# Optimization experiments

Hardware: AMD Instinct MI355X
Metric: run time of the kernel (lower is better)

## Reference

```python
import jax, jax.numpy as jnp
import numpy as np

B, S, F, H = 2, 1024, 1024, 16  # H = n_heads arg; effective chunks Hc = F // H = 64, head_dim = H = 16


def _lin(x, w, b):
    # torch nn.Linear: y = x @ W^T + b, W has shape (out, in)
    return jnp.einsum('bsf,of->bso', x, w) + b


def setup_inputs() -> dict:
    key = jax.random.key(0)
    ks = jax.random.split(key, 16)
    sc = 0.02
    d = {'x': jax.random.normal(ks[0], (B, S, F), jnp.float32)}
    names = ['wq', 'wk', 'wv', 'vq', 'vk', 'vv', 'wo']
    for i, n in enumerate(names):
        d[n + '_w'] = jax.random.normal(ks[1 + 2 * i], (F, F), jnp.float32) * sc
        d[n + '_b'] = jax.random.normal(ks[2 + 2 * i], (F,), jnp.float32) * sc
    return d


def reference(x, wq_w, wq_b, wk_w, wk_b, wv_w, wv_b,
              vq_w, vq_b, vk_w, vk_b, vv_w, vv_b, wo_w, wo_b):
    b, s, f = x.shape
    hc = f // H  # number of chunks produced by torch.split(., n_heads, dim=-1)
    q = _lin(_lin(x, wq_w, wq_b), vq_w, vq_b)
    k = _lin(_lin(x, wk_w, wk_b), vk_w, vk_b)
    v = _lin(_lin(x, wv_w, wv_b), vv_w, vv_b)
    # split into hc chunks of size H along feature dim, concat on batch dim -> (hc, b, s, H)
    q = q.reshape(b, s, hc, H).transpose(2, 0, 1, 3)
    k = k.reshape(b, s, hc, H).transpose(2, 0, 1, 3)
    v = v.reshape(b, s, hc, H).transpose(2, 0, 1, 3)
    scale = jnp.sqrt(jnp.asarray(H, q.dtype))
    scores = jnp.einsum('cbqh,cbkh->cbqk', q, k) / scale  # (hc, b, s, s)
    attn = jax.nn.softmax(scores, axis=-1)
    o = jnp.einsum('cbqk,cbkh->cbqh', attn, v)  # (hc, b, s, H)
    # torch: view(H, b, s, f//H) then unsqueeze(-2).swapaxes(0,-2).reshape(b,s,f)
    o = o.reshape(H, b, s, hc).transpose(1, 2, 0, 3).reshape(b, s, f)
    return _lin(o, wo_w, wo_b)
```

## Files before the change

kernel.cpp:

```cpp
#include <hip/hip_runtime.h>
#include <hip/hip_bf16.h>
#include <stdint.h>

typedef __bf16 bf16_t;
typedef __bf16 bf16x8 __attribute__((ext_vector_type(8)));
typedef __bf16 bf16x4 __attribute__((ext_vector_type(4)));
typedef float f32x4 __attribute__((ext_vector_type(4)));
typedef float f32x16 __attribute__((ext_vector_type(16)));
typedef uint32_t u32x4 __attribute__((ext_vector_type(4)));

#define XN 2097152
#define WN 1048576

typedef __attribute__((address_space(1))) const uint8_t* gas_ptr;
typedef __attribute__((address_space(3))) uint8_t* las_ptr;

static __device__ __forceinline__ uint16_t bfbits(float f) {
    bf16_t b = (bf16_t)f;
    return __builtin_bit_cast(uint16_t, b);
}

__global__ void cast_all_k(const float* __restrict__ x,
    const float* __restrict__ w0, const float* __restrict__ w1, const float* __restrict__ w2,
    const float* __restrict__ w3, const float* __restrict__ w4, const float* __restrict__ w5,
    const float* __restrict__ w6, bf16_t* __restrict__ dst)
{
    const int TOTC = (XN + 7 * WN) / 4;
    for (int c = blockIdx.x * blockDim.x + threadIdx.x; c < TOTC; c += gridDim.x * blockDim.x) {
        int el = c * 4;
        const float* s;
        if (el < XN) {
            s = x + el;
        } else {
            int r = el - XN;
            int wi = r >> 20;
            int off = r & (WN - 1);
            const float* wp = (wi == 0) ? w0 : (wi == 1) ? w1 : (wi == 2) ? w2
                             : (wi == 3) ? w3 : (wi == 4) ? w4 : (wi == 5) ? w5 : w6;
            s = wp + off;
        }
        float4 f = *(const float4*)s;
        bf16x4 o = { (bf16_t)f.x, (bf16_t)f.y, (bf16_t)f.z, (bf16_t)f.w };
        *(bf16x4*)(dst + el) = o;
    }
}

#define QSCALE 0.36067376022224085f

template<int EPI>
__global__ __launch_bounds__(256)
void gemm128(const bf16_t* __restrict__ A0, const bf16_t* __restrict__ A1, const bf16_t* __restrict__ A2,
             const bf16_t* __restrict__ W0, const bf16_t* __restrict__ W1, const bf16_t* __restrict__ W2,
             const float* __restrict__ bias0, const float* __restrict__ bias1, const float* __restrict__ bias2,
             void* O0, void* O1, void* O2)
{
    const int z = blockIdx.z;
    const bf16_t* A = (z == 0) ? A0 : (z == 1) ? A1 : A2;
    const bf16_t* W = (z == 0) ? W0 : (z == 1) ? W1 : W2;
    const float* bias = (z == 0) ? bias0 : (z == 1) ? bias1 : bias2;
    void* Ov = (z == 0) ? O0 : (z == 1) ? O1 : O2;

    __shared__ bf16_t As[128 * 64];
    __shared__ bf16_t Bs[128 * 64];

    const int tid = threadIdx.x;
    const int lane = tid & 63, wave = tid >> 6;
    const int lo = lane & 15, hi = lane >> 4;
    const int wr = wave >> 1, wc = wave & 1;
    const int m0 = blockIdx.y * 128, n0 = blockIdx.x * 128;

    f32x4 acc[4][4] = {};

    for (int kt = 0; kt < 16; ++kt) {
        const int K0 = kt * 64;
        __syncthreads();
#pragma unroll
        for (int i = 0; i < 4; ++i) {
            const int cbase = i * 256 + wave * 64;
            const int c = cbase + lane;
            const int row = c >> 3, ko = c & 7;
            const bf16_t* ga = A + (size_t)(m0 + row) * 1024 + K0 + ko * 8;
            const bf16_t* gb = W + (size_t)(n0 + row) * 1024 + K0 + ko * 8;
            __builtin_amdgcn_global_load_lds((gas_ptr)ga, (las_ptr)(As + cbase * 8), 16, 0, 0);
            __builtin_amdgcn_global_load_lds((gas_ptr)gb, (las_ptr)(Bs + cbase * 8), 16, 0, 0);
        }
        __syncthreads();
#pragma unroll
        for (int kk = 0; kk < 2; ++kk) {
            const int kb = kk * 32 + hi * 8;
            bf16x8 af[4], bfr[4];
#pragma unroll
            for (int m = 0; m < 4; ++m) af[m] = *(const bf16x8*)&As[(wr * 64 + m * 16 + lo) * 64 + kb];
#pragma unroll
            for (int n = 0; n < 4; ++n) bfr[n] = *(const bf16x8*)&Bs[(wc * 64 + n * 16 + lo) * 64 + kb];
#pragma unroll
            for (int m = 0; m < 4; ++m)
#pragma unroll
                for (int n = 0; n < 4; ++n)
                    acc[m][n] = __builtin_amdgcn_mfma_f32_16x16x32_bf16(af[m], bfr[n], acc[m][n], 0, 0, 0);
        }
    }

#pragma unroll
    for (int n = 0; n < 4; ++n) {
        const int col = n0 + wc * 64 + n * 16 + lo;
        const float bv = bias[col];
#pragma unroll
        for (int m = 0; m < 4; ++m) {
            const int r0 = m0 + wr * 64 + m * 16 + hi * 4;
            if (EPI == 2) {
                float* O = (float*)Ov;
#pragma unroll
                for (int r = 0; r < 4; ++r)
                    O[(size_t)(r0 + r) * 1024 + col] = acc[m][n][r] + bv;
            } else if (EPI == 0 || z < 2) {
                bf16_t* O = (bf16_t*)Ov;
                const float sc = (EPI == 1 && z == 0) ? QSCALE : 1.0f;
#pragma unroll
                for (int r = 0; r < 4; ++r)
                    O[(size_t)(r0 + r) * 1024 + col] = (bf16_t)((acc[m][n][r] + bv) * sc);
            } else {
                bf16_t* O = (bf16_t*)Ov;
                int cch = col >> 4, h = col & 15;
                int bb = r0 >> 10, ss = r0 & 1023;
                bf16x4 pv = { (bf16_t)(acc[m][n][0] + bv), (bf16_t)(acc[m][n][1] + bv),
                              (bf16_t)(acc[m][n][2] + bv), (bf16_t)(acc[m][n][3] + bv) };
                *(bf16x4*)(O + ((size_t)((cch * 2 + bb) * 16 + h)) * 1024 + ss) = pv;
            }
        }
    }
}

__global__ __launch_bounds__(256)
void attn_k(const bf16_t* __restrict__ qg, const bf16_t* __restrict__ kg,
            const bf16_t* __restrict__ vtg, bf16_t* __restrict__ y)
{
    const int c = blockIdx.y, b = blockIdx.z;
    const int lane = threadIdx.x & 63, wave = threadIdx.x >> 6;
    const int l31 = lane & 31, hi = lane >> 5;
    const int s = blockIdx.x * 128 + wave * 32 + l31;

    bf16x8 qf = *(const bf16x8*)(qg + ((size_t)(b * 1024 + s)) * 1024 + c * 16 + hi * 8);
    const bf16_t* kptr = kg + ((size_t)(b * 1024 + l31)) * 1024 + c * 16 + hi * 8;
    const bf16_t* vptr = vtg + ((size_t)((c * 2 + b) * 16 + (lane & 15))) * 1024 + hi * 8;

    f32x16 oacc = {};
    const f32x16 z16 = {};
    float den = 0.f;

    bf16x8 kf = *(const bf16x8*)(kptr);
    bf16x8 vf0 = *(const bf16x8*)(vptr);
    bf16x8 vf1 = *(const bf16x8*)(vptr + 16);

#pragma unroll 2
    for (int jt = 0; jt < 32; ++jt) {
        const int jn = (jt + 1) & 31;
        bf16x8 kn  = *(const bf16x8*)(kptr + (size_t)jn * 32768);
        bf16x8 vn0 = *(const bf16x8*)(vptr + jn * 32);
        bf16x8 vn1 = *(const bf16x8*)(vptr + jn * 32 + 16);

        f32x16 st = __builtin_amdgcn_mfma_f32_32x32x16_bf16(kf, qf, z16, 0, 0, 0);

        float p[16];
#pragma unroll
        for (int r = 0; r < 16; ++r) { p[r] = exp2f(st[r]); den += p[r]; }

        uint32_t pk[8];
#pragma unroll
        for (int w = 0; w < 8; ++w)
            pk[w] = (uint32_t)bfbits(p[2 * w]) | ((uint32_t)bfbits(p[2 * w + 1]) << 16);

        uint32_t t0 = hi ? pk[0] : pk[2];
        uint32_t t1 = hi ? pk[1] : pk[3];
        uint32_t t2 = hi ? pk[4] : pk[6];
        uint32_t t3 = hi ? pk[5] : pk[7];
        t0 = (uint32_t)__shfl_xor((int)t0, 32, 64);
        t1 = (uint32_t)__shfl_xor((int)t1, 32, 64);
        t2 = (uint32_t)__shfl_xor((int)t2, 32, 64);
        t3 = (uint32_t)__shfl_xor((int)t3, 32, 64);

        u32x4 f0v, f1v;
        f0v[0] = hi ? t0 : pk[0];  f0v[1] = hi ? t1 : pk[1];
        f0v[2] = hi ? pk[2] : t0;  f0v[3] = hi ? pk[3] : t1;
        f1v[0] = hi ? t2 : pk[4];  f1v[1] = hi ? t3 : pk[5];
        f1v[2] = hi ? pk[6] : t2;  f1v[3] = hi ? pk[7] : t3;
        bf16x8 pf0 = __builtin_bit_cast(bf16x8, f0v);
        bf16x8 pf1 = __builtin_bit_cast(bf16x8, f1v);

        oacc = __builtin_amdgcn_mfma_f32_32x32x16_bf16(vf0, pf0, oacc, 0, 0, 0);
        oacc = __builtin_amdgcn_mfma_f32_32x32x16_bf16(vf1, pf1, oacc, 0, 0, 0);

        kf = kn; vf0 = vn0; vf1 = vn1;
    }

    float dtot = den + __shfl_xor(den, 32, 64);
    float rinv = 1.0f / dtot;

    const int bo = (c >> 1) & 1;
    const int so = (c & 1) * 512 + b * 256 + (s >> 2);
    const int f0i = (c >> 2) * 64 + (s & 3) * 16;
    bf16_t* yb = y + ((size_t)bo * 1024 + so) * 1024 + f0i + 4 * hi;
    bf16x4 o1 = { (bf16_t)(oacc[0] * rinv), (bf16_t)(oacc[1] * rinv),
                  (bf16_t)(oacc[2] * rinv), (bf16_t)(oacc[3] * rinv) };
    *(bf16x4*)(yb) = o1;
    bf16x4 o2 = { (bf16_t)(oacc[4] * rinv), (bf16_t)(oacc[5] * rinv),
                  (bf16_t)(oacc[6] * rinv), (bf16_t)(oacc[7] * rinv) };
    *(bf16x4*)(yb + 8) = o2;
}

extern "C" void kernel_launch(void* const* d_in, const int* in_sizes, int n_in,
                              void* d_out, int out_size, void* d_ws, size_t ws_size,
                              hipStream_t stream)
{
    (void)in_sizes; (void)n_in; (void)out_size; (void)ws_size;
    const float* x    = (const float*)d_in[0];
    const float* wq_b = (const float*)d_in[2];
    const float* wk_b = (const float*)d_in[4];
    const float* wv_b = (const float*)d_in[6];
    const float* vq_b = (const float*)d_in[8];
    const float* vk_b = (const float*)d_in[10];
    const float* vv_b = (const float*)d_in[12];
    const float* wo_b = (const float*)d_in[14];

    bf16_t* base = (bf16_t*)d_ws;
    bf16_t* xbf = base;
    bf16_t* wbf = base + XN;
    bf16_t* q1  = base + XN + 7 * WN;
    bf16_t* k1  = q1 + XN;
    bf16_t* v1  = k1 + XN;
    bf16_t* q   = v1 + XN;
    bf16_t* k   = q + XN;
    bf16_t* vT  = k + XN;
    bf16_t* y   = q1;

    cast_all_k<<<dim3(2048), dim3(256), 0, stream>>>(
        x, (const float*)d_in[1], (const float*)d_in[3], (const float*)d_in[5],
        (const float*)d_in[7], (const float*)d_in[9], (const float*)d_in[11],
        (const float*)d_in[13], base);

    gemm128<0><<<dim3(8, 16, 3), dim3(256), 0, stream>>>(
        xbf, xbf, xbf, wbf, wbf + WN, wbf + 2 * WN,
        wq_b, wk_b, wv_b, q1, k1, v1);

    gemm128<1><<<dim3(8, 16, 3), dim3(256), 0, stream>>>(
        q1, k1, v1, wbf + 3 * WN, wbf + 4 * WN, wbf + 5 * WN,
        vq_b, vk_b, vv_b, q, k, vT);

    attn_k<<<dim3(8, 64, 2), dim3(256), 0, stream>>>(q, k, vT, y);

    gemm128<2><<<dim3(8, 16, 1), dim3(256), 0, stream>>>(
        y, y, y, wbf + 6 * WN, wbf + 6 * WN, wbf + 6 * WN,
        wo_b, wo_b, wo_b, d_out, d_out, d_out);
}
```

Baseline: 229.8 us.

## Stage K/V in LDS with fragment layout, shrink GEMM tiles, swizzle block order

The GEMMs switch from 128x128 to 128x64 tiles on a 1D grid with an XCD-aware block swizzle, which doubles block count for better CU fill and L2 locality. The second GEMM now writes K and V directly in an MFMA-fragment-ready layout. The attention kernel loads each chunk's whole K and V into LDS once per 512-thread block instead of streaming them per wave from global memory. It also replaces the shuffle-based P repacking with v_permlane32_swap and uses the raw exp2 builtin. The risks are heavier LDS use (64KB per block) limiting occupancy and the complexity of the custom layouts.

New measurement: 199.9 us. -13.0%, faster.

```diff
diff --git a/kernel.cpp b/kernel.cpp
--- a/kernel.cpp
+++ b/kernel.cpp
@@ -54,22 +54,30 @@
              const float* __restrict__ bias0, const float* __restrict__ bias1, const float* __restrict__ bias2,
              void* O0, void* O1, void* O2)
 {
-    const int z = blockIdx.z;
+    const int bid = blockIdx.x;
+    int z, mt, nt;
+    if (EPI < 2) {
+        const int swz = (bid & 7) * 96 + (bid >> 3);
+        z = swz >> 8; mt = (swz >> 4) & 15; nt = swz & 15;
+    } else {
+        const int swz = (bid & 7) * 32 + (bid >> 3);
+        z = 0; mt = swz >> 4; nt = swz & 15;
+    }
     const bf16_t* A = (z == 0) ? A0 : (z == 1) ? A1 : A2;
     const bf16_t* W = (z == 0) ? W0 : (z == 1) ? W1 : W2;
     const float* bias = (z == 0) ? bias0 : (z == 1) ? bias1 : bias2;
     void* Ov = (z == 0) ? O0 : (z == 1) ? O1 : O2;
 
     __shared__ bf16_t As[128 * 64];
-    __shared__ bf16_t Bs[128 * 64];
+    __shared__ bf16_t Bs[64 * 64];
 
     const int tid = threadIdx.x;
     const int lane = tid & 63, wave = tid >> 6;
     const int lo = lane & 15, hi = lane >> 4;
     const int wr = wave >> 1, wc = wave & 1;
-    const int m0 = blockIdx.y * 128, n0 = blockIdx.x * 128;
-
-    f32x4 acc[4][4] = {};
+    const int m0 = mt * 128, n0 = nt * 64;
+
+    f32x4 acc[4][2] = {};
 
     for (int kt = 0; kt < 16; ++kt) {
         const int K0 = kt * 64;
@@ -80,30 +88,36 @@
             const int c = cbase + lane;
             const int row = c >> 3, ko = c & 7;
             const bf16_t* ga = A + (size_t)(m0 + row) * 1024 + K0 + ko * 8;
+            __builtin_amdgcn_global_load_lds((gas_ptr)ga, (las_ptr)(As + cbase * 8), 16, 0, 0);
+        }
+#pragma unroll
+        for (int i = 0; i < 2; ++i) {
+            const int cbase = i * 256 + wave * 64;
+            const int c = cbase + lane;
+            const int row = c >> 3, ko = c & 7;
             const bf16_t* gb = W + (size_t)(n0 + row) * 1024 + K0 + ko * 8;
-            __builtin_amdgcn_global_load_lds((gas_ptr)ga, (las_ptr)(As + cbase * 8), 16, 0, 0);
             __builtin_amdgcn_global_load_lds((gas_ptr)gb, (las_ptr)(Bs + cbase * 8), 16, 0, 0);
         }
         __syncthreads();
 #pragma unroll
         for (int kk = 0; kk < 2; ++kk) {
             const int kb = kk * 32 + hi * 8;
-            bf16x8 af[4], bfr[4];
+            bf16x8 af[4], bfr[2];
 #pragma unroll
             for (int m = 0; m < 4; ++m) af[m] = *(const bf16x8*)&As[(wr * 64 + m * 16 + lo) * 64 + kb];
 #pragma unroll
-            for (int n = 0; n < 4; ++n) bfr[n] = *(const bf16x8*)&Bs[(wc * 64 + n * 16 + lo) * 64 + kb];
+            for (int n = 0; n < 2; ++n) bfr[n] = *(const bf16x8*)&Bs[(wc * 32 + n * 16 + lo) * 64 + kb];
 #pragma unroll
             for (int m = 0; m < 4; ++m)
 #pragma unroll
-                for (int n = 0; n < 4; ++n)
+                for (int n = 0; n < 2; ++n)
                     acc[m][n] = __builtin_amdgcn_mfma_f32_16x16x32_bf16(af[m], bfr[n], acc[m][n], 0, 0, 0);
         }
     }
 
 #pragma unroll
-    for (int n = 0; n < 4; ++n) {
-        const int col = n0 + wc * 64 + n * 16 + lo;
+    for (int n = 0; n < 2; ++n) {
+        const int col = n0 + wc * 32 + n * 16 + lo;
         const float bv = bias[col];
 #pragma unroll
         for (int m = 0; m < 4; ++m) {
@@ -113,84 +127,97 @@
 #pragma unroll
                 for (int r = 0; r < 4; ++r)
                     O[(size_t)(r0 + r) * 1024 + col] = acc[m][n][r] + bv;
-            } else if (EPI == 0 || z < 2) {
+            } else if (EPI == 0 || z == 0) {
                 bf16_t* O = (bf16_t*)Ov;
-                const float sc = (EPI == 1 && z == 0) ? QSCALE : 1.0f;
+                const float sc = (EPI == 1) ? QSCALE : 1.0f;
 #pragma unroll
                 for (int r = 0; r < 4; ++r)
                     O[(size_t)(r0 + r) * 1024 + col] = (bf16_t)((acc[m][n][r] + bv) * sc);
+            } else if (z == 1) {
+                bf16_t* O = (bf16_t*)Ov;
+                const int cch = col >> 4, h = col & 15;
+                const int bb = r0 >> 10;
+                const size_t sb = (size_t)(cch * 2 + bb) * 16384;
+#pragma unroll
+                for (int r = 0; r < 4; ++r) {
+                    const int ss = (r0 + r) & 1023;
+                    const int C = ((ss >> 5) << 6) + ((h >> 3) << 5) + (ss & 31);
+                    O[sb + C * 8 + (h & 7)] = (bf16_t)(acc[m][n][r] + bv);
+                }
             } else {
                 bf16_t* O = (bf16_t*)Ov;
-                int cch = col >> 4, h = col & 15;
-                int bb = r0 >> 10, ss = r0 & 1023;
+                const int cch = col >> 4, h = col & 15;
+                const int bb = r0 >> 10;
+                const int s0 = r0 & 1023;
+                const int C = ((s0 >> 5) << 6) + (((s0 >> 4) & 1) << 5) + (((s0 >> 3) & 1) << 4) + h;
                 bf16x4 pv = { (bf16_t)(acc[m][n][0] + bv), (bf16_t)(acc[m][n][1] + bv),
                               (bf16_t)(acc[m][n][2] + bv), (bf16_t)(acc[m][n][3] + bv) };
-                *(bf16x4*)(O + ((size_t)((cch * 2 + bb) * 16 + h)) * 1024 + ss) = pv;
+                *(bf16x4*)(O + (size_t)(cch * 2 + bb) * 16384 + C * 8 + (s0 & 7)) = pv;
             }
         }
     }
 }
 
-__global__ __launch_bounds__(256)
-void attn_k(const bf16_t* __restrict__ qg, const bf16_t* __restrict__ kg,
-            const bf16_t* __restrict__ vtg, bf16_t* __restrict__ y)
-{
+__global__ __launch_bounds__(512)
+void attn_k(const bf16_t* __restrict__ qg, const bf16_t* __restrict__ kfr,
+            const bf16_t* __restrict__ vfr, bf16_t* __restrict__ y)
+{
+    __shared__ bf16_t lds[32768];
+
     const int c = blockIdx.y, b = blockIdx.z;
-    const int lane = threadIdx.x & 63, wave = threadIdx.x >> 6;
+    const int tid = threadIdx.x;
+    const int lane = tid & 63, wave = tid >> 6;
     const int l31 = lane & 31, hi = lane >> 5;
-    const int s = blockIdx.x * 128 + wave * 32 + l31;
+    const int s = blockIdx.x * 256 + wave * 32 + l31;
+
+    const bf16_t* kb = kfr + (size_t)(c * 2 + b) * 16384;
+    const bf16_t* vb = vfr + (size_t)(c * 2 + b) * 16384;
+#pragma unroll
+    for (int i = 0; i < 4; ++i) {
+        const int cbase = i * 512 + wave * 64;
+        __builtin_amdgcn_global_load_lds((gas_ptr)(kb + (cbase + lane) * 8),
+                                         (las_ptr)((uint8_t*)lds + cbase * 16), 16, 0, 0);
+        __builtin_amdgcn_global_load_lds((gas_ptr)(vb + (cbase + lane) * 8),
+                                         (las_ptr)((uint8_t*)lds + 32768 + cbase * 16), 16, 0, 0);
+    }
 
     bf16x8 qf = *(const bf16x8*)(qg + ((size_t)(b * 1024 + s)) * 1024 + c * 16 + hi * 8);
-    const bf16_t* kptr = kg + ((size_t)(b * 1024 + l31)) * 1024 + c * 16 + hi * 8;
-    const bf16_t* vptr = vtg + ((size_t)((c * 2 + b) * 16 + (lane & 15))) * 1024 + hi * 8;
+
+    __syncthreads();
 
     f32x16 oacc = {};
     const f32x16 z16 = {};
     float den = 0.f;
-
-    bf16x8 kf = *(const bf16x8*)(kptr);
-    bf16x8 vf0 = *(const bf16x8*)(vptr);
-    bf16x8 vf1 = *(const bf16x8*)(vptr + 16);
-
-#pragma unroll 2
+    const int vslot = ((lane >> 5) * 16 + (lane & 15)) * 8;
+
     for (int jt = 0; jt < 32; ++jt) {
-        const int jn = (jt + 1) & 31;
-        bf16x8 kn  = *(const bf16x8*)(kptr + (size_t)jn * 32768);
-        bf16x8 vn0 = *(const bf16x8*)(vptr + jn * 32);
-        bf16x8 vn1 = *(const bf16x8*)(vptr + jn * 32 + 16);
+        bf16x8 kf  = *(const bf16x8*)&lds[jt * 512 + lane * 8];
+        bf16x8 vf0 = *(const bf16x8*)&lds[16384 + jt * 512 + vslot];
+        bf16x8 vf1 = *(const bf16x8*)&lds[16384 + jt * 512 + 256 + vslot];
 
         f32x16 st = __builtin_amdgcn_mfma_f32_32x32x16_bf16(kf, qf, z16, 0, 0, 0);
 
         float p[16];
 #pragma unroll
-        for (int r = 0; r < 16; ++r) { p[r] = exp2f(st[r]); den += p[r]; }
+        for (int r = 0; r < 16; ++r) { p[r] = __builtin_amdgcn_exp2f(st[r]); den += p[r]; }
 
         uint32_t pk[8];
 #pragma unroll
         for (int w = 0; w < 8; ++w)
             pk[w] = (uint32_t)bfbits(p[2 * w]) | ((uint32_t)bfbits(p[2 * w + 1]) << 16);
 
-        uint32_t t0 = hi ? pk[0] : pk[2];
-        uint32_t t1 = hi ? pk[1] : pk[3];
-        uint32_t t2 = hi ? pk[4] : pk[6];
-        uint32_t t3 = hi ? pk[5] : pk[7];
-        t0 = (uint32_t)__shfl_xor((int)t0, 32, 64);
-        t1 = (uint32_t)__shfl_xor((int)t1, 32, 64);
-        t2 = (uint32_t)__shfl_xor((int)t2, 32, 64);
-        t3 = (uint32_t)__shfl_xor((int)t3, 32, 64);
-
-        u32x4 f0v, f1v;
-        f0v[0] = hi ? t0 : pk[0];  f0v[1] = hi ? t1 : pk[1];
-        f0v[2] = hi ? pk[2] : t0;  f0v[3] = hi ? pk[3] : t1;
-        f1v[0] = hi ? t2 : pk[4];  f1v[1] = hi ? t3 : pk[5];
-        f1v[2] = hi ? pk[6] : t2;  f1v[3] = hi ? pk[7] : t3;
+        asm("v_permlane32_swap_b32 %0, %1" : "+v"(pk[0]), "+v"(pk[2]));
+        asm("v_permlane32_swap_b32 %0, %1" : "+v"(pk[1]), "+v"(pk[3]));
+        asm("v_permlane32_swap_b32 %0, %1" : "+v"(pk[4]), "+v"(pk[6]));
+        asm("v_permlane32_swap_b32 %0, %1" : "+v"(pk[5]), "+v"(pk[7]));
+
+        u32x4 f0v = { pk[0], pk[1], pk[2], pk[3] };
+        u32x4 f1v = { pk[4], pk[5], pk[6], pk[7] };
         bf16x8 pf0 = __builtin_bit_cast(bf16x8, f0v);
         bf16x8 pf1 = __builtin_bit_cast(bf16x8, f1v);
 
         oacc = __builtin_amdgcn_mfma_f32_32x32x16_bf16(vf0, pf0, oacc, 0, 0, 0);
         oacc = __builtin_amdgcn_mfma_f32_32x32x16_bf16(vf1, pf1, oacc, 0, 0, 0);
-
-        kf = kn; vf0 = vn0; vf1 = vn1;
     }
 
     float dtot = den + __shfl_xor(den, 32, 64);
@@ -229,8 +256,8 @@
     bf16_t* k1  = q1 + XN;
     bf16_t* v1  = k1 + XN;
     bf16_t* q   = v1 + XN;
-    bf16_t* k   = q + XN;
-    bf16_t* vT  = k + XN;
+    bf16_t* kc  = q + XN;
+    bf16_t* vc  = kc + XN;
     bf16_t* y   = q1;
 
     cast_all_k<<<dim3(2048), dim3(256), 0, stream>>>(
@@ -238,17 +265,17 @@
         (const float*)d_in[7], (const float*)d_in[9], (const float*)d_in[11],
         (const float*)d_in[13], base);
 
-    gemm128<0><<<dim3(8, 16, 3), dim3(256), 0, stream>>>(
+    gemm128<0><<<dim3(768), dim3(256), 0, stream>>>(
         xbf, xbf, xbf, wbf, wbf + WN, wbf + 2 * WN,
         wq_b, wk_b, wv_b, q1, k1, v1);
 
-    gemm128<1><<<dim3(8, 16, 3), dim3(256), 0, stream>>>(
+    gemm128<1><<<dim3(768), dim3(256), 0, stream>>>(
         q1, k1, v1, wbf + 3 * WN, wbf + 4 * WN, wbf + 5 * WN,
-        vq_b, vk_b, vv_b, q, k, vT);
-
-    attn_k<<<dim3(8, 64, 2), dim3(256), 0, stream>>>(q, k, vT, y);
-
-    gemm128<2><<<dim3(8, 16, 1), dim3(256), 0, stream>>>(
+        vq_b, vk_b, vv_b, q, kc, vc);
+
+    attn_k<<<dim3(4, 64, 2), dim3(512), 0, stream>>>(q, kc, vc, y);
+
+    gemm128<2><<<dim3(256), dim3(256), 0, stream>>>(
         y, y, y, wbf + 6 * WN, wbf + 6 * WN, wbf + 6 * WN,
         wo_b, wo_b, wo_b, d_out, d_out, d_out);
 }
```
